# Kernel optimization log

Measured on AMD Instinct MI355X. Metric: run time of the kernel, lower is better.

The kernel has to match this reference:

```python
import jax, jax.numpy as jnp
import numpy as np

H = 32          # num_attention_heads
D_NOPE = 128    # qk_nope_head_dim
D_ROPE = 64     # qk_rope_head_dim
D_Q = D_NOPE + D_ROPE  # 192, q_head_dim
D_V = 128       # v_head_dim
R_KV = 512      # kv_lora_rank
EPS = 1e-6


def setup_inputs() -> dict:
    key = jax.random.key(0)
    ks = jax.random.split(key, 5)
    return {
        "hidden_states": jax.random.normal(ks[0], (2, 4096, 4096), jnp.float32),
        "q_a_w": jax.random.normal(ks[1], (1536, 4096), jnp.float32) * 0.02,
        "q_b_w": jax.random.normal(ks[2], (H * D_Q, 1536), jnp.float32) * 0.02,
        "kv_a_w": jax.random.normal(ks[3], (R_KV + D_ROPE, 4096), jnp.float32) * 0.02,
        "kv_b_w": jax.random.normal(ks[4], (H * (D_NOPE + D_V), R_KV), jnp.float32) * 0.02,
        "q_a_ln_w": jnp.ones((1536,), jnp.float32),
        "kv_a_ln_w": jnp.ones((R_KV,), jnp.float32),
    }


def _rmsnorm(x, w):
    xf = x.astype(jnp.float32)
    var = jnp.mean(xf * xf, axis=-1, keepdims=True)
    return (w * (xf * jax.lax.rsqrt(var + EPS))).astype(x.dtype)


def _deepseek_transpose(x):
    # interleave swap on last dim: view (..., d//2, 2) -> transpose -> (..., d)
    b, h, s, d = x.shape
    return x.reshape(b, h, s, d // 2, 2).swapaxes(-1, -2).reshape(b, h, s, d)


def reference(hidden_states, q_a_w, q_b_w, kv_a_w, kv_b_w, q_a_ln_w, kv_a_ln_w):
    b, s, _ = hidden_states.shape
    # Q path: low-rank A -> RMSNorm -> B
    q = _rmsnorm(hidden_states @ q_a_w.T, q_a_ln_w) @ q_b_w.T
    q = q.reshape(b, s, H, D_Q).transpose(0, 2, 1, 3)  # [b, H, s, 192]
    q_nope, q_pe = q[..., :D_NOPE], q[..., D_NOPE:]
    # KV path: joint A proj, split compressed_kv / k_pe
    ckv = hidden_states @ kv_a_w.T                      # [b, s, 576]
    compressed_kv, k_pe = ckv[..., :R_KV], ckv[..., R_KV:]
    k_pe = k_pe.reshape(b, s, 1, D_ROPE).transpose(0, 2, 1, 3)  # [b, 1, s, 64]
    kv = _rmsnorm(compressed_kv, kv_a_ln_w) @ kv_b_w.T
    kv = kv.reshape(b, s, H, D_NOPE + D_V).transpose(0, 2, 1, 3)  # [b, H, s, 256]
    k_nope, value_states = kv[..., :D_NOPE], kv[..., D_NOPE:]
    # interleaved rope transpose
    q_pe = _deepseek_transpose(q_pe)
    k_pe = _deepseek_transpose(k_pe)
    query_states = jnp.concatenate([q_nope, q_pe], axis=-1)                     # [b, H, s, 192]
    key_states = jnp.concatenate(
        [k_nope, jnp.broadcast_to(k_pe, (b, H, s, D_ROPE))], axis=-1)           # [b, H, s, 192]
    v_padded = jnp.pad(value_states, ((0, 0), (0, 0), (0, 0), (0, D_Q - D_V)))  # [b, H, s, 192]
    return jnp.concatenate([query_states, key_states, v_padded], axis=1)        # [b, 3H, s, 192]
```

## Files before the change

### kernel.cpp

```cpp
#include <hip/hip_runtime.h>
#include <hip/hip_bf16.h>

typedef __hip_bfloat16 bf16;
typedef __attribute__((ext_vector_type(8))) short short8;
typedef __attribute__((ext_vector_type(4))) float floatx4;

struct bf16x4 { bf16 a, b, c, d; };

#define OUT_BSTRIDE 75497472u
#define OUT_HSTRIDE 786432u

__device__ __forceinline__ void gload_lds16(const bf16* g, bf16* l) {
    __builtin_amdgcn_global_load_lds((const __attribute__((address_space(1))) void*)g,
                                     (__attribute__((address_space(3))) void*)l,
                                     16, 0, 0);
}

__global__ __launch_bounds__(256) void cvt_f32_bf16(const float* __restrict__ src,
                                                    bf16* __restrict__ dst, int n4) {
    const int stride = gridDim.x * blockDim.x;
    for (int i = blockIdx.x * blockDim.x + threadIdx.x; i < n4; i += stride) {
        const float4 v = ((const float4*)src)[i];
        bf16x4 o;
        o.a = __float2bfloat16(v.x);
        o.b = __float2bfloat16(v.y);
        o.c = __float2bfloat16(v.z);
        o.d = __float2bfloat16(v.w);
        ((bf16x4*)dst)[i] = o;
    }
}

template <int MODE>
__global__ __launch_bounds__(256) void gemm_bt(const bf16* __restrict__ A,
                                               const bf16* __restrict__ Bq,
                                               const bf16* __restrict__ Bkv,
                                               bf16* __restrict__ Cq,
                                               bf16* __restrict__ Ckv,
                                               float* __restrict__ Of) {
    constexpr int K   = (MODE == 0) ? 4096 : (MODE == 1) ? 1536 : 512;
    constexpr int LDA = (MODE == 0) ? 4096 : (MODE == 1) ? 1536 : 576;
    constexpr int LDB = (MODE == 0) ? 4096 : (MODE == 1) ? 1536 : 512;

    __shared__ __align__(16) bf16 sA[128 * 32];
    __shared__ __align__(16) bf16 sB[128 * 32];

    const int tid = threadIdx.x;
    const int m0  = blockIdx.x * 128;

    const bf16* Bsel;
    bf16* Cbf = nullptr;
    int n0, nmax = 0x40000000, ldc = 0;
    if constexpr (MODE == 0) {
        if (blockIdx.y < 12) {
            Bsel = Bq;  n0 = blockIdx.y * 128;        nmax = 1536; ldc = 1536; Cbf = Cq;
        } else {
            Bsel = Bkv; n0 = (blockIdx.y - 12) * 128; nmax = 576;  ldc = 576;  Cbf = Ckv;
        }
    } else {
        Bsel = Bq; n0 = blockIdx.y * 128;
    }

    const int r0 = tid >> 2;
    const int kc = tid & 3;
    const bf16* ga0 = A + (size_t)(m0 + r0) * LDA + kc * 8;
    const bf16* ga1 = ga0 + (size_t)64 * LDA;
    int br0 = n0 + r0;      if (br0 > nmax - 1) br0 = nmax - 1;
    int br1 = n0 + r0 + 64; if (br1 > nmax - 1) br1 = nmax - 1;
    const bf16* gb0 = Bsel + (size_t)br0 * LDB + kc * 8;
    const bf16* gb1 = Bsel + (size_t)br1 * LDB + kc * 8;
    bf16* lA0 = sA + tid * 8;
    bf16* lA1 = sA + (tid + 256) * 8;
    bf16* lB0 = sB + tid * 8;
    bf16* lB1 = sB + (tid + 256) * 8;

    const int lane = tid & 63;
    const int wid  = tid >> 6;
    const int wm   = wid >> 1;
    const int wn   = wid & 1;
    const int ln   = lane & 15;
    const int qo   = (lane >> 4) * 8;

    const short8* pa[4];
    const short8* pb[4];
#pragma unroll
    for (int i = 0; i < 4; ++i) {
        pa[i] = (const short8*)(sA + (wm * 64 + i * 16 + ln) * 32 + qo);
        pb[i] = (const short8*)(sB + (wn * 64 + i * 16 + ln) * 32 + qo);
    }

    floatx4 acc[4][4];
#pragma unroll
    for (int i = 0; i < 4; ++i)
#pragma unroll
        for (int j = 0; j < 4; ++j) acc[i][j] = (floatx4){0.f, 0.f, 0.f, 0.f};

    for (int k0 = 0; k0 < K; k0 += 32) {
        gload_lds16(ga0, lA0);
        gload_lds16(ga1, lA1);
        gload_lds16(gb0, lB0);
        gload_lds16(gb1, lB1);
        ga0 += 32; ga1 += 32; gb0 += 32; gb1 += 32;
        __syncthreads();

        short8 af[4], bfr[4];
#pragma unroll
        for (int i = 0; i < 4; ++i) af[i] = *pa[i];
#pragma unroll
        for (int j = 0; j < 4; ++j) bfr[j] = *pb[j];
#pragma unroll
        for (int i = 0; i < 4; ++i)
#pragma unroll
            for (int j = 0; j < 4; ++j)
                acc[i][j] = __builtin_amdgcn_mfma_f32_16x16x32_bf16(af[i], bfr[j], acc[i][j], 0, 0, 0);
        __syncthreads();
    }

    const int rowq = (lane >> 4) * 4;
#pragma unroll
    for (int j = 0; j < 4; ++j) {
        const int c0 = n0 + wn * 64 + j * 16;
        const int c  = c0 + ln;

        if constexpr (MODE == 0) {
            const bool ok = (c < nmax);
#pragma unroll
            for (int i = 0; i < 4; ++i) {
                const int t = m0 + wm * 64 + i * 16 + rowq;
#pragma unroll
                for (int r = 0; r < 4; ++r) {
                    if (ok) Cbf[(size_t)(t + r) * ldc + c] = __float2bfloat16(acc[i][j][r]);
                }
            }
        } else {
            size_t colbase;
            if constexpr (MODE == 1) {
                const int h  = c0 / 192;
                const int e0 = c0 - h * 192;
                const int e  = e0 + ln;
                int d;
                if (e0 >= 128) {
                    const int p = e - 128;
                    d = 128 + (p & 1) * 32 + (p >> 1);
                } else {
                    d = e;
                }
                colbase = (size_t)h * OUT_HSTRIDE + d;
            } else {
                const int h  = c0 >> 8;
                const int e0 = c0 & 255;
                const int e  = e0 + ln;
                const int head = (e0 < 128) ? (32 + h) : (64 + h);
                const int d    = (e0 < 128) ? e : (e - 128);
                colbase = (size_t)head * OUT_HSTRIDE + d;
            }
#pragma unroll
            for (int i = 0; i < 4; ++i) {
                const int tbase = m0 + wm * 64 + i * 16 + rowq;
#pragma unroll
                for (int r = 0; r < 4; ++r) {
                    const int t  = tbase + r;
                    const int bb = t >> 12;
                    const int ss = t & 4095;
                    Of[(size_t)bb * OUT_BSTRIDE + (size_t)ss * 192 + colbase] = acc[i][j][r];
                }
            }
        }
    }
}

__global__ __launch_bounds__(256) void norm_kpe(bf16* __restrict__ q_a,
                                                bf16* __restrict__ ckv,
                                                const float* __restrict__ qw,
                                                const float* __restrict__ kw,
                                                float* __restrict__ out) {
    __shared__ float red[4];
    __shared__ float skpe[64];
    const int tid = threadIdx.x;
    const int r   = blockIdx.x;

    if (r < 8192) {
        bf16* row = q_a + (size_t)r * 1536;
        float x[6];
#pragma unroll
        for (int k = 0; k < 6; ++k) x[k] = __bfloat162float(row[tid + k * 256]);
        float ss = 0.f;
#pragma unroll
        for (int k = 0; k < 6; ++k) ss += x[k] * x[k];
#pragma unroll
        for (int o = 32; o > 0; o >>= 1) ss += __shfl_down(ss, o, 64);
        if ((tid & 63) == 0) red[tid >> 6] = ss;
        __syncthreads();
        const float tot   = red[0] + red[1] + red[2] + red[3];
        const float scale = rsqrtf(tot * (1.0f / 1536.0f) + 1e-6f);
#pragma unroll
        for (int k = 0; k < 6; ++k) {
            const float w = qw[tid + k * 256];
            row[tid + k * 256] = __float2bfloat16(x[k] * scale * w);
        }
    } else {
        const int t = r - 8192;
        bf16* row   = ckv + (size_t)t * 576;
        float x0 = __bfloat162float(row[tid]);
        float x1 = __bfloat162float(row[tid + 256]);
        if (tid < 64) skpe[tid] = __bfloat162float(row[512 + tid]);
        float ss = x0 * x0 + x1 * x1;
#pragma unroll
        for (int o = 32; o > 0; o >>= 1) ss += __shfl_down(ss, o, 64);
        if ((tid & 63) == 0) red[tid >> 6] = ss;
        __syncthreads();
        const float tot   = red[0] + red[1] + red[2] + red[3];
        const float scale = rsqrtf(tot * (1.0f / 512.0f) + 1e-6f);
        row[tid]       = __float2bfloat16(x0 * scale * kw[tid]);
        row[tid + 256] = __float2bfloat16(x1 * scale * kw[tid + 256]);

        const int i  = tid & 63;
        const int hg = tid >> 6;
        const float v = skpe[2 * (i & 31) + (i >> 5)];
        const int bb  = t >> 12;
        const int ssx = t & 4095;
        float* obase = out + (size_t)bb * OUT_BSTRIDE + (size_t)ssx * 192 + 128 + i;
#pragma unroll
        for (int h = 0; h < 8; ++h) {
            const int head = hg * 8 + h;
            obase[(size_t)(32 + head) * OUT_HSTRIDE] = v;
            obase[(size_t)(64 + head) * OUT_HSTRIDE] = 0.0f;
        }
    }
}

extern "C" void kernel_launch(void* const* d_in, const int* in_sizes, int n_in,
                              void* d_out, int out_size, void* d_ws, size_t ws_size,
                              hipStream_t stream) {
    const float* hidden = (const float*)d_in[0];
    const float* q_a_w  = (const float*)d_in[1];
    const float* q_b_w  = (const float*)d_in[2];
    const float* kv_a_w = (const float*)d_in[3];
    const float* kv_b_w = (const float*)d_in[4];
    const float* q_ln   = (const float*)d_in[5];
    const float* kv_ln  = (const float*)d_in[6];
    float* out = (float*)d_out;

    bf16* hid_b  = (bf16*)d_ws;
    bf16* qaw_b  = hid_b + (size_t)8192 * 4096;
    bf16* qbw_b  = qaw_b + (size_t)1536 * 4096;
    bf16* kvaw_b = qbw_b + (size_t)6144 * 1536;
    bf16* kvbw_b = kvaw_b + (size_t)576 * 4096;
    bf16* q_a    = kvbw_b + (size_t)8192 * 512;
    bf16* ckv    = q_a + (size_t)8192 * 1536;

    dim3 blk(256);
    cvt_f32_bf16<<<dim3(4096), blk, 0, stream>>>(hidden, hid_b, 8192 * 4096 / 4);
    cvt_f32_bf16<<<dim3(1024), blk, 0, stream>>>(q_a_w, qaw_b, 1536 * 4096 / 4);
    cvt_f32_bf16<<<dim3(1024), blk, 0, stream>>>(q_b_w, qbw_b, 6144 * 1536 / 4);
    cvt_f32_bf16<<<dim3(512),  blk, 0, stream>>>(kv_a_w, kvaw_b, 576 * 4096 / 4);
    cvt_f32_bf16<<<dim3(512),  blk, 0, stream>>>(kv_b_w, kvbw_b, 8192 * 512 / 4);

    gemm_bt<0><<<dim3(64, 17), blk, 0, stream>>>(hid_b, qaw_b, kvaw_b, q_a, ckv, nullptr);
    norm_kpe<<<dim3(16384), blk, 0, stream>>>(q_a, ckv, q_ln, kv_ln, out);
    gemm_bt<1><<<dim3(64, 48), blk, 0, stream>>>(q_a, qbw_b, nullptr, nullptr, nullptr, out);
    gemm_bt<2><<<dim3(64, 64), blk, 0, stream>>>(ckv, kvbw_b, nullptr, nullptr, nullptr, out);
}
```

Baseline: 1.229 ms.

## Add 256x256 double-buffered 8-wave GEMM for q_b and kv_b projections

```diff
diff --git a/kernel.cpp b/kernel.cpp
--- a/kernel.cpp
+++ b/kernel.cpp
@@ -37,9 +37,9 @@
                                                bf16* __restrict__ Cq,
                                                bf16* __restrict__ Ckv,
                                                float* __restrict__ Of) {
-    constexpr int K   = (MODE == 0) ? 4096 : (MODE == 1) ? 1536 : 512;
-    constexpr int LDA = (MODE == 0) ? 4096 : (MODE == 1) ? 1536 : 576;
-    constexpr int LDB = (MODE == 0) ? 4096 : (MODE == 1) ? 1536 : 512;
+    constexpr int K   = 4096;
+    constexpr int LDA = 4096;
+    constexpr int LDB = 4096;
 
     __shared__ __align__(16) bf16 sA[128 * 32];
     __shared__ __align__(16) bf16 sB[128 * 32];
@@ -50,14 +50,10 @@
     const bf16* Bsel;
     bf16* Cbf = nullptr;
     int n0, nmax = 0x40000000, ldc = 0;
-    if constexpr (MODE == 0) {
-        if (blockIdx.y < 12) {
-            Bsel = Bq;  n0 = blockIdx.y * 128;        nmax = 1536; ldc = 1536; Cbf = Cq;
-        } else {
-            Bsel = Bkv; n0 = (blockIdx.y - 12) * 128; nmax = 576;  ldc = 576;  Cbf = Ckv;
-        }
+    if (blockIdx.y < 12) {
+        Bsel = Bq;  n0 = blockIdx.y * 128;        nmax = 1536; ldc = 1536; Cbf = Cq;
     } else {
-        Bsel = Bq; n0 = blockIdx.y * 128;
+        Bsel = Bkv; n0 = (blockIdx.y - 12) * 128; nmax = 576;  ldc = 576;  Cbf = Ckv;
     }
 
     const int r0 = tid >> 2;
@@ -120,49 +116,205 @@
     for (int j = 0; j < 4; ++j) {
         const int c0 = n0 + wn * 64 + j * 16;
         const int c  = c0 + ln;
-
-        if constexpr (MODE == 0) {
-            const bool ok = (c < nmax);
-#pragma unroll
-            for (int i = 0; i < 4; ++i) {
-                const int t = m0 + wm * 64 + i * 16 + rowq;
-#pragma unroll
-                for (int r = 0; r < 4; ++r) {
-                    if (ok) Cbf[(size_t)(t + r) * ldc + c] = __float2bfloat16(acc[i][j][r]);
-                }
-            }
+        const bool ok = (c < nmax);
+#pragma unroll
+        for (int i = 0; i < 4; ++i) {
+            const int t = m0 + wm * 64 + i * 16 + rowq;
+#pragma unroll
+            for (int r = 0; r < 4; ++r) {
+                if (ok) Cbf[(size_t)(t + r) * ldc + c] = __float2bfloat16(acc[i][j][r]);
+            }
+        }
+    }
+}
+
+template <int MODE>
+__global__ __launch_bounds__(512) void gemm8(const bf16* __restrict__ A,
+                                             const bf16* __restrict__ B,
+                                             float* __restrict__ Of) {
+    constexpr int K   = (MODE == 1) ? 1536 : 512;
+    constexpr int LDA = (MODE == 1) ? 1536 : 576;
+    constexpr int LDB = (MODE == 1) ? 1536 : 512;
+    constexpr int NT  = K / 64;
+
+    __shared__ __align__(16) bf16 sA[2][2][128 * 64];
+    __shared__ __align__(16) bf16 sB[2][2][128 * 64];
+
+    const int tid = threadIdx.x;
+    const int m0  = blockIdx.x * 256;
+    const int n0  = blockIdx.y * 256;
+
+    const int srow   = tid >> 3;
+    const int schunk = (tid & 7) ^ (srow & 7);
+    const bf16* gA0 = A + (size_t)(m0 + srow) * LDA + schunk * 8;
+    const bf16* gA1 = gA0 + (size_t)64 * LDA;
+    const bf16* gB0 = B + (size_t)(n0 + srow) * LDB + schunk * 8;
+    const bf16* gB1 = gB0 + (size_t)64 * LDB;
+
+    auto stageA = [&](int bb, int h, int k0) {
+        bf16* d = &sA[bb][h][tid * 8];
+        const size_t ho = (size_t)h * (128 * LDA) + k0;
+        gload_lds16(gA0 + ho, d);
+        gload_lds16(gA1 + ho, d + 4096);
+    };
+    auto stageB = [&](int bb, int h, int k0) {
+        bf16* d = &sB[bb][h][tid * 8];
+        const size_t ho = (size_t)h * (128 * LDB) + k0;
+        gload_lds16(gB0 + ho, d);
+        gload_lds16(gB1 + ho, d + 4096);
+    };
+
+    const int lane = tid & 63;
+    const int wid  = tid >> 6;
+    const int wm   = wid >> 2;
+    const int wn   = wid & 3;
+    const int ln   = lane & 15;
+    const int q4   = lane >> 4;
+    const int swz  = ln & 7;
+    const int aoff0 = ln * 64 + ((q4 ^ swz) * 8);
+    const int aoff1 = ln * 64 + (((4 + q4) ^ swz) * 8);
+
+    floatx4 acc[8][4];
+#pragma unroll
+    for (int i = 0; i < 8; ++i)
+#pragma unroll
+        for (int j = 0; j < 4; ++j) acc[i][j] = (floatx4){0.f, 0.f, 0.f, 0.f};
+
+    stageA(0, 0, 0);  stageA(0, 1, 0);
+    stageB(0, 0, 0);  stageB(0, 1, 0);
+    stageA(1, 0, 64); stageA(1, 1, 64);
+    asm volatile("s_waitcnt vmcnt(4)" ::: "memory");
+    __builtin_amdgcn_s_barrier();
+    asm volatile("" ::: "memory");
+
+    short8 a0[4][2], a1[4][2], b0[2][2], b1[2][2];
+
+    for (int c = 0; c < NT; ++c) {
+        const int bb = c & 1;
+        const bf16* hA = &sA[bb][wm][0];
+        const bf16* hB = &sB[bb][wn >> 1][(wn & 1) * 4096];
+        const int kn1 = (c + 1) * 64;
+        const int kn2 = (c + 2) * 64;
+
+#pragma unroll
+        for (int i = 0; i < 4; ++i) {
+            a0[i][0] = *(const short8*)(hA + i * 1024 + aoff0);
+            a0[i][1] = *(const short8*)(hA + i * 1024 + aoff1);
+        }
+#pragma unroll
+        for (int j = 0; j < 2; ++j) {
+            b0[j][0] = *(const short8*)(hB + j * 1024 + aoff0);
+            b0[j][1] = *(const short8*)(hB + j * 1024 + aoff1);
+        }
+        if (c + 1 < NT) stageB(bb ^ 1, 0, kn1);
+        __builtin_amdgcn_s_barrier();
+        asm volatile("s_waitcnt lgkmcnt(0)" ::: "memory");
+        __builtin_amdgcn_s_setprio(1);
+#pragma unroll
+        for (int i = 0; i < 4; ++i)
+#pragma unroll
+            for (int j = 0; j < 2; ++j) {
+                acc[i][j] = __builtin_amdgcn_mfma_f32_16x16x32_bf16(a0[i][0], b0[j][0], acc[i][j], 0, 0, 0);
+                acc[i][j] = __builtin_amdgcn_mfma_f32_16x16x32_bf16(a0[i][1], b0[j][1], acc[i][j], 0, 0, 0);
+            }
+        __builtin_amdgcn_s_setprio(0);
+        __builtin_amdgcn_s_barrier();
+        asm volatile("" ::: "memory");
+
+#pragma unroll
+        for (int i = 0; i < 4; ++i) {
+            a1[i][0] = *(const short8*)(hA + 4096 + i * 1024 + aoff0);
+            a1[i][1] = *(const short8*)(hA + 4096 + i * 1024 + aoff1);
+        }
+        if (c + 1 < NT) stageB(bb ^ 1, 1, kn1);
+        __builtin_amdgcn_s_barrier();
+        asm volatile("s_waitcnt lgkmcnt(0)" ::: "memory");
+        __builtin_amdgcn_s_setprio(1);
+#pragma unroll
+        for (int i = 0; i < 4; ++i)
+#pragma unroll
+            for (int j = 0; j < 2; ++j) {
+                acc[4 + i][j] = __builtin_amdgcn_mfma_f32_16x16x32_bf16(a1[i][0], b0[j][0], acc[4 + i][j], 0, 0, 0);
+                acc[4 + i][j] = __builtin_amdgcn_mfma_f32_16x16x32_bf16(a1[i][1], b0[j][1], acc[4 + i][j], 0, 0, 0);
+            }
+        __builtin_amdgcn_s_setprio(0);
+        __builtin_amdgcn_s_barrier();
+        asm volatile("" ::: "memory");
+
+#pragma unroll
+        for (int j = 0; j < 2; ++j) {
+            b1[j][0] = *(const short8*)(hB + (2 + j) * 1024 + aoff0);
+            b1[j][1] = *(const short8*)(hB + (2 + j) * 1024 + aoff1);
+        }
+        if (c + 2 < NT) stageA(bb, 0, kn2);
+        __builtin_amdgcn_s_barrier();
+        asm volatile("s_waitcnt lgkmcnt(0)" ::: "memory");
+        __builtin_amdgcn_s_setprio(1);
+#pragma unroll
+        for (int i = 0; i < 4; ++i)
+#pragma unroll
+            for (int j = 0; j < 2; ++j) {
+                acc[i][2 + j] = __builtin_amdgcn_mfma_f32_16x16x32_bf16(a0[i][0], b1[j][0], acc[i][2 + j], 0, 0, 0);
+                acc[i][2 + j] = __builtin_amdgcn_mfma_f32_16x16x32_bf16(a0[i][1], b1[j][1], acc[i][2 + j], 0, 0, 0);
+            }
+        __builtin_amdgcn_s_setprio(0);
+        __builtin_amdgcn_s_barrier();
+        asm volatile("" ::: "memory");
+
+        if (c + 2 < NT) stageA(bb, 1, kn2);
+        __builtin_amdgcn_s_barrier();
+        asm volatile("s_waitcnt lgkmcnt(0)" ::: "memory");
+        __builtin_amdgcn_s_setprio(1);
+#pragma unroll
+        for (int i = 0; i < 4; ++i)
+#pragma unroll
+            for (int j = 0; j < 2; ++j) {
+                acc[4 + i][2 + j] = __builtin_amdgcn_mfma_f32_16x16x32_bf16(a1[i][0], b1[j][0], acc[4 + i][2 + j], 0, 0, 0);
+                acc[4 + i][2 + j] = __builtin_amdgcn_mfma_f32_16x16x32_bf16(a1[i][1], b1[j][1], acc[4 + i][2 + j], 0, 0, 0);
+            }
+        __builtin_amdgcn_s_setprio(0);
+        if (c + 2 < NT) {
+            asm volatile("s_waitcnt vmcnt(4)" ::: "memory");
+        } else if (c + 1 < NT) {
+            asm volatile("s_waitcnt vmcnt(0)" ::: "memory");
+        }
+        __builtin_amdgcn_s_barrier();
+        asm volatile("" ::: "memory");
+    }
+
+#pragma unroll
+    for (int nj = 0; nj < 4; ++nj) {
+        const int c0 = n0 + wn * 64 + nj * 16;
+        size_t colbase;
+        if constexpr (MODE == 1) {
+            const int h  = c0 / 192;
+            const int e0 = c0 - h * 192;
+            const int e  = e0 + ln;
+            int d;
+            if (e0 >= 128) {
+                const int p = e - 128;
+                d = 128 + (p & 1) * 32 + (p >> 1);
+            } else {
+                d = e;
+            }
+            colbase = (size_t)h * OUT_HSTRIDE + d;
         } else {
-            size_t colbase;
-            if constexpr (MODE == 1) {
-                const int h  = c0 / 192;
-                const int e0 = c0 - h * 192;
-                const int e  = e0 + ln;
-                int d;
-                if (e0 >= 128) {
-                    const int p = e - 128;
-                    d = 128 + (p & 1) * 32 + (p >> 1);
-                } else {
-                    d = e;
-                }
-                colbase = (size_t)h * OUT_HSTRIDE + d;
-            } else {
-                const int h  = c0 >> 8;
-                const int e0 = c0 & 255;
-                const int e  = e0 + ln;
-                const int head = (e0 < 128) ? (32 + h) : (64 + h);
-                const int d    = (e0 < 128) ? e : (e - 128);
-                colbase = (size_t)head * OUT_HSTRIDE + d;
-            }
-#pragma unroll
-            for (int i = 0; i < 4; ++i) {
-                const int tbase = m0 + wm * 64 + i * 16 + rowq;
-#pragma unroll
-                for (int r = 0; r < 4; ++r) {
-                    const int t  = tbase + r;
-                    const int bb = t >> 12;
-                    const int ss = t & 4095;
-                    Of[(size_t)bb * OUT_BSTRIDE + (size_t)ss * 192 + colbase] = acc[i][j][r];
-                }
+            const int h  = c0 >> 8;
+            const int e0 = c0 & 255;
+            const int e  = e0 + ln;
+            const int head = (e0 < 128) ? (32 + h) : (64 + h);
+            const int d    = (e0 < 128) ? e : (e - 128);
+            colbase = (size_t)head * OUT_HSTRIDE + d;
+        }
+#pragma unroll
+        for (int mi = 0; mi < 8; ++mi) {
+            const int tbase = m0 + wm * 128 + mi * 16 + q4 * 4;
+#pragma unroll
+            for (int r = 0; r < 4; ++r) {
+                const int t  = tbase + r;
+                const int b2 = t >> 12;
+                const int ss = t & 4095;
+                Of[(size_t)b2 * OUT_BSTRIDE + (size_t)ss * 192 + colbase] = acc[mi][nj][r];
             }
         }
     }
@@ -249,6 +401,7 @@
     bf16* ckv    = q_a + (size_t)8192 * 1536;
 
     dim3 blk(256);
+    dim3 blk8(512);
     cvt_f32_bf16<<<dim3(4096), blk, 0, stream>>>(hidden, hid_b, 8192 * 4096 / 4);
     cvt_f32_bf16<<<dim3(1024), blk, 0, stream>>>(q_a_w, qaw_b, 1536 * 4096 / 4);
     cvt_f32_bf16<<<dim3(1024), blk, 0, stream>>>(q_b_w, qbw_b, 6144 * 1536 / 4);
@@ -257,6 +410,6 @@
 
     gemm_bt<0><<<dim3(64, 17), blk, 0, stream>>>(hid_b, qaw_b, kvaw_b, q_a, ckv, nullptr);
     norm_kpe<<<dim3(16384), blk, 0, stream>>>(q_a, ckv, q_ln, kv_ln, out);
-    gemm_bt<1><<<dim3(64, 48), blk, 0, stream>>>(q_a, qbw_b, nullptr, nullptr, nullptr, out);
-    gemm_bt<2><<<dim3(64, 64), blk, 0, stream>>>(ckv, kvbw_b, nullptr, nullptr, nullptr, out);
-}
+    gemm8<1><<<dim3(32, 24), blk8, 0, stream>>>(q_a, qbw_b, out);
+    gemm8<2><<<dim3(32, 32), blk8, 0, stream>>>(ckv, kvbw_b, out);
+}
```

Result: no change. 1.234 ms (+0.4%).
